# Performance work log

Hardware: AMD Instinct MI355X
Metric: run time of the kernel (lower is better)

The kernel has to match this reference:

```python
import jax, jax.numpy as jnp
import numpy as np

N_FREQ = 128
N_SPACE = 3
DIS_DIM = 2 * N_FREQ * N_SPACE  # 768


def sin_emb(x):
    # x: [E, 3] -> [E, 768]; frequencies = 2*pi*arange(n_freq) as in DiffCSP SinusoidsEmbedding
    freq = 2.0 * jnp.pi * jnp.arange(N_FREQ, dtype=x.dtype)
    e = (x[..., None] * freq).reshape(x.shape[0], N_SPACE * N_FREQ)
    return jnp.concatenate([jnp.sin(e), jnp.cos(e)], axis=-1)


def layer_norm(x, g, b, eps=1e-5):
    m = jnp.mean(x, axis=-1, keepdims=True)
    v = jnp.var(x, axis=-1, keepdims=True)
    return (x - m) * jax.lax.rsqrt(v + eps) * g + b


def setup_inputs() -> dict:
    key = jax.random.key(0)
    ks = jax.random.split(key, 16)
    N, E, B, H = 10000, 200000, 50, 512
    E_IN = 2 * H + DIS_DIM + 6  # 1798
    s = 0.02
    return {
        "node_features": jax.random.normal(ks[0], (N, H), jnp.float32),
        "lattices": jax.random.normal(ks[1], (B, 6), jnp.float32),
        "edge_index": jax.random.randint(ks[2], (2, E), 0, N),
        "edge2graph": jax.random.randint(ks[3], (E,), 0, B),
        "frac_diff": jax.random.uniform(ks[4], (E, 3), jnp.float32),
        "num_atoms": jax.random.randint(ks[5], (B,), 1, 200),
        "ln_gamma": jnp.ones((H,), jnp.float32),
        "ln_beta": jnp.zeros((H,), jnp.float32),
        "W_e1": jax.random.normal(ks[6], (E_IN, H), jnp.float32) * s,
        "b_e1": jnp.zeros((H,), jnp.float32),
        "W_e2": jax.random.normal(ks[7], (H, H), jnp.float32) * s,
        "b_e2": jnp.zeros((H,), jnp.float32),
        "W_n1": jax.random.normal(ks[8], (2 * H, H), jnp.float32) * s,
        "b_n1": jnp.zeros((H,), jnp.float32),
        "W_n2": jax.random.normal(ks[9], (H, H), jnp.float32) * s,
        "b_n2": jnp.zeros((H,), jnp.float32),
    }


def reference(node_features, lattices, edge_index, edge2graph, frac_diff, num_atoms,
              ln_gamma, ln_beta, W_e1, b_e1, W_e2, b_e2, W_n1, b_n1, W_n2, b_n2):
    N = node_features.shape[0]
    # pre-LN (ln=True): residual uses raw input
    h = layer_norm(node_features, ln_gamma, ln_beta)
    # edge model: gather + concat + 2-layer MLP with SiLU
    hi = h[edge_index[0]]
    hj = h[edge_index[1]]
    fd = sin_emb(frac_diff)
    lat_e = lattices.reshape(lattices.shape[0], -1)[edge2graph]
    e_in = jnp.concatenate([hi, hj, lat_e, fd], axis=1)  # [E, 1798]
    e = jax.nn.silu(e_in @ W_e1 + b_e1)
    e = jax.nn.silu(e @ W_e2 + b_e2)
    # node model: scatter-mean over edge source + 2-layer MLP
    agg = jax.ops.segment_sum(e, edge_index[0], num_segments=N)
    cnt = jax.ops.segment_sum(jnp.ones((e.shape[0],), e.dtype), edge_index[0], num_segments=N)
    agg = agg / jnp.maximum(cnt, 1.0)[:, None]
    n_in = jnp.concatenate([h, agg], axis=1)  # [N, 1024]
    o = jax.nn.silu(n_in @ W_n1 + b_n1)
    o = jax.nn.silu(o @ W_n2 + b_n2)
    return node_features + o
```

## Files before the change

### kernel.cpp

```cpp
#include <hip/hip_runtime.h>
#include <hip/hip_bf16.h>


#include <type_traits>

typedef __attribute__((ext_vector_type(8))) short bfrag;
typedef __attribute__((ext_vector_type(4))) float ffrag;

#define DEVI __device__ __forceinline__

constexpr int N_NODES = 10000;
constexpr int N_EDGES = 200000;
constexpr int HD      = 512;
constexpr int NT      = HD / 16;
constexpr int SLABW   = 520;
constexpr int KSTR    = NT * 64 * 8;

DEVI float silu_f(float v) {
    return v * __builtin_amdgcn_rcpf(1.0f + __expf(-v));
}

DEVI ushort f2bf(float f) {
    unsigned u = __float_as_uint(f);
    unsigned r = (u + 0x7fffu + ((u >> 16) & 1u)) >> 16;
    return (ushort)r;
}
DEVI float bf2f(ushort v) { return __uint_as_float((unsigned)v << 16); }

DEVI int cperm(int col) {
    return (col & ~63) | ((col & 15) << 2) | ((col >> 4) & 3);
}

__global__ void wswz_kernel(const float* __restrict__ W, ushort* __restrict__ dst,
                            int Kp, int mode) {
    int fid = blockIdx.x * blockDim.x + threadIdx.x;
    int total = (Kp / 32) * NT * 64;
    if (fid >= total) return;
    int l  = fid & 63;
    int nn = (fid >> 6) & 31;
    int kk = fid >> 11;
    int col = nn * 16 + (l & 15);
    int kb  = kk * 32 + (l >> 4) * 8;
    union { ushort u16[8]; uint4 u4; } v;
    for (int j = 0; j < 8; ++j) {
        int krow = kb + j;
        int src;
        if (mode == 3) {
            int d = krow >> 8, rm = krow & 255, k = rm >> 1;
            src = ((rm & 1) ? 1414 : 1030) + d * 128 + k;
        } else if (mode == 1) {
            src = (krow & ~63) | ((krow & 3) << 4) | ((krow >> 2) & 15);
        } else {
            src = krow;
        }
        v.u16[j] = f2bf(W[(size_t)src * HD + col]);
    }
    *(uint4*)(dst + (size_t)fid * 8) = v.u4;
}

__global__ void ln_kernel(const float* __restrict__ x, const float* __restrict__ g,
                          const float* __restrict__ b, ushort* __restrict__ h) {
    __shared__ float wred[8];
    __shared__ float mb[2];
    int row = blockIdx.x;
    int t = threadIdx.x;
    const float* xr = x + (size_t)row * HD;
    float2 xv = *(const float2*)(xr + 2 * t);
    float s = xv.x + xv.y, qq = xv.x * xv.x + xv.y * xv.y;
    for (int o = 32; o; o >>= 1) { s += __shfl_down(s, o); qq += __shfl_down(qq, o); }
    int w = t >> 6, l = t & 63;
    if (l == 0) { wred[w] = s; wred[w + 4] = qq; }
    __syncthreads();
    if (t == 0) {
        float S = wred[0] + wred[1] + wred[2] + wred[3];
        float Q = wred[4] + wred[5] + wred[6] + wred[7];
        float m = S * (1.0f / HD);
        float v = Q * (1.0f / HD) - m * m;
        mb[0] = m; mb[1] = rsqrtf(v + 1e-5f);
    }
    __syncthreads();
    float m = mb[0], rs = mb[1];
    float2 gv = *(const float2*)(g + 2 * t);
    float2 bv = *(const float2*)(b + 2 * t);
    __hip_bfloat162 o2 = __float22bfloat162_rn(
        float2{(xv.x - m) * rs * gv.x + bv.x, (xv.y - m) * rs * gv.y + bv.y});
    *(__hip_bfloat162*)(h + (size_t)row * HD + 2 * t) = o2;
}

__global__ void latb_kernel(const float* __restrict__ latt, const float* __restrict__ W_e1,
                            const float* __restrict__ b1, float* __restrict__ LATBp) {
    int g = blockIdx.x;
    int t = threadIdx.x;
    float a = b1[t];
    for (int c = 0; c < 6; ++c)
        a += latt[g * 6 + c] * W_e1[(size_t)(1024 + c) * HD + t];
    LATBp[(size_t)g * HD + cperm(t)] = a;
}

__global__ void zero_kernel(int* __restrict__ c32, float4* __restrict__ agg4) {
    int i = blockIdx.x * 256 + threadIdx.x;
    if (i < N_NODES) c32[i] = 0;
    agg4[i] = float4{0.f, 0.f, 0.f, 0.f};
}

__global__ void hist_kernel(const int* __restrict__ eidx, int* __restrict__ cnt32) {
    int e = blockIdx.x * 256 + threadIdx.x;
    if (e < N_EDGES) atomicAdd(&cnt32[eidx[e]], 1);
}

__global__ void scan_kernel(const int* __restrict__ cnt32, int* __restrict__ row_ptr,
                            int* __restrict__ cursor) {
    __shared__ int buf[1024];
    int t = threadIdx.x;
    int base = t * 10;
    int loc[10]; int s = 0;
    for (int i = 0; i < 10; ++i) {
        int idx = base + i;
        int v = (idx < N_NODES) ? cnt32[idx] : 0;
        loc[i] = s; s += v;
    }
    buf[t] = s; __syncthreads();
    for (int off = 1; off < 1024; off <<= 1) {
        int v = 0; if (t >= off) v = buf[t - off];
        __syncthreads();
        buf[t] += v; __syncthreads();
    }
    int excl = buf[t] - s;
    for (int i = 0; i < 10; ++i) {
        int idx = base + i;
        if (idx < N_NODES) { int p = excl + loc[i]; row_ptr[idx] = p; cursor[idx] = p; }
    }
    if (t == 0) row_ptr[N_NODES] = N_EDGES;
}

__global__ void csr_fill(const int* __restrict__ eidx, int* __restrict__ cursor,
                         int* __restrict__ ebuf) {
    int e = blockIdx.x * 256 + threadIdx.x;
    if (e >= N_EDGES) return;
    int pos = atomicAdd(&cursor[eidx[e]], 1);
    ebuf[pos] = e;
}

__global__ void aggdiv_kernel(const float* __restrict__ agg, const int* __restrict__ rp,
                              ushort* __restrict__ aggb) {
    int i = blockIdx.x * 256 + threadIdx.x;
    int row = i >> 8;
    int deg = rp[row + 1] - rp[row];
    float rc = __builtin_amdgcn_rcpf((float)max(deg, 1));
    float2 v = *(const float2*)(agg + (size_t)i * 2);
    *(__hip_bfloat162*)(aggb + (size_t)i * 2) =
        __float22bfloat162_rn(float2{v.x * rc, v.y * rc});
}

__global__ void sentinel_kernel(float* o, int n) {
    int i = blockIdx.x * 256 + threadIdx.x;
    if (i < n) o[i] = 123456789.0f;
}

template <int KTN, int MT>
DEVI void kloop_rot(ffrag (&acc)[MT][4], const ushort* sl, const ushort* bp0,
                    int ml, int q) {
    bfrag b_[4];
    const ushort* bp = bp0;
    #pragma unroll
    for (int n = 0; n < 4; ++n) b_[n] = *(const bfrag*)(bp + n * 512);
    #pragma unroll
    for (int p = 0; p < KTN; ++p) {
        bfrag a_[MT];
        #pragma unroll
        for (int m = 0; m < MT; ++m)
            a_[m] = *(const bfrag*)&sl[(16 * m + ml) * SLABW + p * 32 + q * 8];
        const ushort* bpn = bp + KSTR;
        #pragma unroll
        for (int n = 0; n < 4; ++n) {
            #pragma unroll
            for (int m = 0; m < MT; ++m)
                acc[m][n] = __builtin_amdgcn_mfma_f32_16x16x32_bf16(a_[m], b_[n], acc[m][n], 0, 0, 0);
            if (p + 1 < KTN) b_[n] = *(const bfrag*)(bpn + n * 512);
        }
        bp = bpn;
    }
}

__global__ __launch_bounds__(512, 4) void hab_gemm(
    const ushort* __restrict__ h, const ushort* __restrict__ w1a_s,
    const ushort* __restrict__ w1b_s, ushort* __restrict__ HAp,
    ushort* __restrict__ HBp) {

    __shared__ __align__(16) ushort slab[32 * SLABW];
    const int t = threadIdx.x;
    const int w = t >> 6;
    const int l = t & 63;
    const int q = l >> 4;
    const int ml = l & 15;
    const int rowbase = blockIdx.x * 32;
    const ushort* Bswz = blockIdx.y ? w1b_s : w1a_s;
    ushort* out = blockIdx.y ? HBp : HAp;

    for (int j = 0; j < 4; ++j) {
        int rr = w * 4 + j;
        int row = rowbase + rr;
        if (row >= N_NODES) row = N_NODES - 1;
        *(uint4*)&slab[rr * SLABW + l * 8] =
            *(const uint4*)(h + (size_t)row * HD + l * 8);
    }
    __syncthreads();

    ffrag acc[2][4];
    for (int m = 0; m < 2; ++m)
        for (int n = 0; n < 4; ++n)
            acc[m][n] = (ffrag){0.f, 0.f, 0.f, 0.f};

    kloop_rot<16, 2>(acc, slab, Bswz + ((size_t)(w << 2) * 64 + l) * 8, ml, q);

    for (int m = 0; m < 2; ++m)
        for (int rr = 0; rr < 4; ++rr) {
            int grow = rowbase + 16 * m + 4 * q + rr;
            if (grow < N_NODES) {
                union { __hip_bfloat162 h2[2]; ushort4 u4; } pk;
                pk.h2[0] = __float22bfloat162_rn(float2{acc[m][0][rr], acc[m][1][rr]});
                pk.h2[1] = __float22bfloat162_rn(float2{acc[m][2][rr], acc[m][3][rr]});
                *(ushort4*)(out + (size_t)grow * HD + w * 64 + ml * 4) = pk.u4;
            }
        }
}

__global__ __launch_bounds__(512, 4) void edge_mlp(
    const ushort* __restrict__ HAp,   const ushort* __restrict__ HBp,
    const float* __restrict__ LATBp,  const ushort* __restrict__ w1c,
    const ushort* __restrict__ w2s,   const float* __restrict__ b2,
    float* __restrict__ agg,
    const int* __restrict__ edge_index, const int* __restrict__ e2g,
    const float* __restrict__ frac_diff, const int* __restrict__ ebuf) {

    __shared__ __align__(16) ushort slab[64 * SLABW];
    __shared__ int   ssrc[64];
    __shared__ int   sdst[64];
    __shared__ int   sgrp[64];
    __shared__ float sfd[64 * 3];

    const int t = threadIdx.x;
    const int w = t >> 6;
    const int l = t & 63;
    const int q = l >> 4;
    const int ml = l & 15;
    const int rowbase = blockIdx.x * 64;

    if (t < 64) {
        int eid = ebuf[rowbase + t];
        ssrc[t] = edge_index[eid];
        sdst[t] = edge_index[N_EDGES + eid];
        sgrp[t] = e2g[eid];
        for (int c = 0; c < 3; ++c) sfd[t * 3 + c] = frac_diff[(size_t)eid * 3 + c];
    }
    __syncthreads();

    ffrag acc[4][4];
    {
        const int cb = w * 64 + ml * 4;
        for (int m = 0; m < 4; ++m)
            for (int rr = 0; rr < 4; ++rr) {
                int rowl = 16 * m + 4 * q + rr;
                ushort4 a4 = *(const ushort4*)(HAp + (size_t)ssrc[rowl] * HD + cb);
                ushort4 h4 = *(const ushort4*)(HBp + (size_t)sdst[rowl] * HD + cb);
                float4  l4 = *(const float4*)(LATBp + (size_t)sgrp[rowl] * HD + cb);
                acc[m][0][rr] = bf2f(a4.x) + bf2f(h4.x) + l4.x;
                acc[m][1][rr] = bf2f(a4.y) + bf2f(h4.y) + l4.y;
                acc[m][2][rr] = bf2f(a4.z) + bf2f(h4.z) + l4.z;
                acc[m][3][rr] = bf2f(a4.w) + bf2f(h4.w) + l4.w;
            }
    }

    const int r  = t >> 3;
    const int c0 = (t & 7) * 4;
    float fd3[3] = { sfd[r * 3 + 0], sfd[r * 3 + 1], sfd[r * 3 + 2] };

    auto stage = [&](int phase) {
        float s = 0.f, c = 0.f, sx = 0.f, cx = 0.f, s16 = 0.f, c16 = 0.f;
        int dcur = -1;
        #pragma unroll
        for (int i = 0; i < 12; ++i) {
            int cc = c0 + 32 * i;
            int cp = phase * 384 + cc;
            int d = cp >> 8;
            if (d != dcur) {
                dcur = d;
                float x = fd3[d];
                float rx = __builtin_amdgcn_fractf(x);
                sx  = __builtin_amdgcn_sinf(rx);
                cx  = __builtin_amdgcn_cosf(rx);
                float r16 = __builtin_amdgcn_fractf(16.0f * x);
                s16 = __builtin_amdgcn_sinf(r16);
                c16 = __builtin_amdgcn_cosf(r16);
                int k0 = (cp & 255) >> 1;
                float r0 = __builtin_amdgcn_fractf((float)k0 * x);
                s = __builtin_amdgcn_sinf(r0);
                c = __builtin_amdgcn_cosf(r0);
            } else {
                float ns = s * c16 + c * s16;
                float nc = c * c16 - s * s16;
                s = ns; c = nc;
            }
            float s1 = s * cx + c * sx;
            float c1 = c * cx - s * sx;
            union { __hip_bfloat162 h2[2]; ushort4 u4; } pk;
            pk.h2[0] = __float22bfloat162_rn(float2{s, c});
            pk.h2[1] = __float22bfloat162_rn(float2{s1, c1});
            *(ushort4*)&slab[r * SLABW + cc] = pk.u4;
        }
    };

    const ushort* bpw1 = w1c + ((size_t)(w << 2) * 64 + l) * 8;
    const ushort* bpw2 = w2s + ((size_t)(w << 2) * 64 + l) * 8;

    stage(0);
    __syncthreads();
    kloop_rot<12, 4>(acc, slab, bpw1, ml, q);
    __syncthreads();
    stage(1);
    __syncthreads();
    kloop_rot<12, 4>(acc, slab, bpw1 + (size_t)12 * KSTR, ml, q);
    __syncthreads();

    for (int m = 0; m < 4; ++m)
        for (int rr = 0; rr < 4; ++rr) {
            int rowl = 16 * m + 4 * q + rr;
            union { __hip_bfloat162 h2[2]; ushort4 u4; } pk;
            pk.h2[0] = __float22bfloat162_rn(
                float2{silu_f(acc[m][0][rr]), silu_f(acc[m][1][rr])});
            pk.h2[1] = __float22bfloat162_rn(
                float2{silu_f(acc[m][2][rr]), silu_f(acc[m][3][rr])});
            *(ushort4*)&slab[rowl * SLABW + w * 64 + ml * 4] = pk.u4;
        }
    for (int m = 0; m < 4; ++m)
        for (int n = 0; n < 4; ++n)
            acc[m][n] = (ffrag){0.f, 0.f, 0.f, 0.f};
    __syncthreads();

    kloop_rot<16, 4>(acc, slab, bpw2, ml, q);

    float* fs = (float*)slab;
    for (int hh = 0; hh < 2; ++hh) {
        __syncthreads();
        if ((w >> 2) == hh) {
            for (int n = 0; n < 4; ++n) {
                int cg = w * 64 + n * 16 + ml;
                int lc = cg - hh * 256;
                float bv = b2[cg];
                for (int m = 0; m < 4; ++m)
                    for (int rr = 0; rr < 4; ++rr) {
                        int rowl = 16 * m + 4 * q + rr;
                        fs[rowl * 256 + lc] = silu_f(acc[m][n][rr] + bv);
                    }
            }
        }
        __syncthreads();
        if (t < 256) {
            int col = hh * 256 + t;
            int cur = ssrc[0];
            float run = 0.f;
            for (int rr2 = 0; rr2 < 64; ++rr2) {
                int nd = ssrc[rr2];
                if (nd != cur) {
                    unsafeAtomicAdd(&agg[(size_t)cur * HD + col], run);
                    run = 0.f; cur = nd;
                }
                run += fs[rr2 * 256 + t];
            }
            unsafeAtomicAdd(&agg[(size_t)cur * HD + col], run);
        }
    }
}

__global__ __launch_bounds__(512, 4) void node_mlp(
    const ushort* __restrict__ h,     const ushort* __restrict__ aggb,
    const ushort* __restrict__ wn1s,  const ushort* __restrict__ wn2s,
    const float* __restrict__ b1,     const float* __restrict__ b2,
    const float* __restrict__ nf,     float* __restrict__ out) {

    __shared__ __align__(16) ushort slab[32 * SLABW];

    const int t = threadIdx.x;
    const int w = t >> 6;
    const int l = t & 63;
    const int q = l >> 4;
    const int ml = l & 15;
    const int rowbase = blockIdx.x * 32;

    ffrag acc[2][4];
    for (int m = 0; m < 2; ++m)
        for (int n = 0; n < 4; ++n)
            acc[m][n] = (ffrag){0.f, 0.f, 0.f, 0.f};

    auto load_rows = [&](const ushort* base) {
        for (int j = 0; j < 4; ++j) {
            int rr = w * 4 + j;
            int row = rowbase + rr;
            if (row >= N_NODES) row = N_NODES - 1;
            *(uint4*)&slab[rr * SLABW + l * 8] =
                *(const uint4*)(base + (size_t)row * HD + l * 8);
        }
    };
    const ushort* bp1 = wn1s + ((size_t)(w << 2) * 64 + l) * 8;
    const ushort* bp2 = wn2s + ((size_t)(w << 2) * 64 + l) * 8;

    load_rows(h);                        __syncthreads();
    kloop_rot<16, 2>(acc, slab, bp1, ml, q);
    __syncthreads();
    load_rows(aggb);                     __syncthreads();
    kloop_rot<16, 2>(acc, slab, bp1 + (size_t)16 * KSTR, ml, q);
    __syncthreads();

    {
        float bv[4];
        for (int n = 0; n < 4; ++n) bv[n] = b1[w * 64 + n * 16 + ml];
        for (int m = 0; m < 2; ++m)
            for (int rr = 0; rr < 4; ++rr) {
                int rowl = 16 * m + 4 * q + rr;
                union { __hip_bfloat162 h2[2]; ushort4 u4; } pk;
                pk.h2[0] = __float22bfloat162_rn(
                    float2{silu_f(acc[m][0][rr] + bv[0]), silu_f(acc[m][1][rr] + bv[1])});
                pk.h2[1] = __float22bfloat162_rn(
                    float2{silu_f(acc[m][2][rr] + bv[2]), silu_f(acc[m][3][rr] + bv[3])});
                *(ushort4*)&slab[rowl * SLABW + w * 64 + ml * 4] = pk.u4;
            }
    }
    for (int m = 0; m < 2; ++m)
        for (int n = 0; n < 4; ++n)
            acc[m][n] = (ffrag){0.f, 0.f, 0.f, 0.f};
    __syncthreads();

    kloop_rot<16, 2>(acc, slab, bp2, ml, q);

    for (int n = 0; n < 4; ++n) {
        int cg = w * 64 + n * 16 + ml;
        float bv = b2[cg];
        for (int m = 0; m < 2; ++m)
            for (int rr = 0; rr < 4; ++rr) {
                int rowl = 16 * m + 4 * q + rr;
                int row = rowbase + rowl;
                if (row < N_NODES) {
                    float v = silu_f(acc[m][n][rr] + bv);
                    out[(size_t)row * HD + cg] = nf[(size_t)row * HD + cg] + v;
                }
            }
    }
}

extern "C" void kernel_launch(void* const* d_in, const int* in_sizes, int n_in,
                              void* d_out, int out_size, void* d_ws, size_t ws_size,
                              hipStream_t stream) {
    const float* nf      = (const float*)d_in[0];
    const float* latt    = (const float*)d_in[1];
    const int*   eidx    = (const int*)d_in[2];
    const int*   e2g     = (const int*)d_in[3];
    const float* fd      = (const float*)d_in[4];
    const float* ln_g    = (const float*)d_in[6];
    const float* ln_b    = (const float*)d_in[7];
    const float* W_e1    = (const float*)d_in[8];
    const float* b_e1    = (const float*)d_in[9];
    const float* W_e2    = (const float*)d_in[10];
    const float* b_e2    = (const float*)d_in[11];
    const float* W_n1    = (const float*)d_in[12];
    const float* b_n1    = (const float*)d_in[13];
    const float* W_n2    = (const float*)d_in[14];
    const float* b_n2    = (const float*)d_in[15];
    float* out = (float*)d_out;

    auto al = [](size_t x) { return (x + 511) & ~(size_t)511; };
    size_t off_h    = 0;                         size_t sz_h    = (size_t)N_NODES * HD * 2;
    size_t off_w1a  = al(off_h + sz_h);          size_t sz_w1a  = (size_t)HD * HD * 2;
    size_t off_w1b  = al(off_w1a + sz_w1a);      size_t sz_w1b  = (size_t)HD * HD * 2;
    size_t off_w1c  = al(off_w1b + sz_w1b);      size_t sz_w1c  = (size_t)768 * HD * 2;
    size_t off_w2   = al(off_w1c + sz_w1c);      size_t sz_w2   = (size_t)HD * HD * 2;
    size_t off_wn1  = al(off_w2 + sz_w2);        size_t sz_wn1  = (size_t)2 * HD * HD * 2;
    size_t off_wn2  = al(off_wn1 + sz_wn1);      size_t sz_wn2  = (size_t)HD * HD * 2;
    size_t off_ha   = al(off_wn2 + sz_wn2);      size_t sz_ha   = (size_t)N_NODES * HD * 2;
    size_t off_hb   = al(off_ha + sz_ha);        size_t sz_hb   = (size_t)N_NODES * HD * 2;
    size_t off_lb   = al(off_hb + sz_hb);        size_t sz_lb   = (size_t)50 * HD * 4;
    size_t off_agb  = al(off_lb + sz_lb);        size_t sz_agb  = (size_t)N_NODES * HD * 2;
    size_t off_c32  = al(off_agb + sz_agb);      size_t sz_c32  = (size_t)N_NODES * 4;
    size_t off_cur  = al(off_c32 + sz_c32);      size_t sz_cur  = (size_t)N_NODES * 4;
    size_t off_rp   = al(off_cur + sz_cur);      size_t sz_rp   = (size_t)(N_NODES + 1) * 4;
    size_t off_ebuf = al(off_rp + sz_rp);        size_t sz_ebuf = (size_t)N_EDGES * 4;
    size_t off_agg  = al(off_ebuf + sz_ebuf);    size_t sz_agg  = (size_t)N_NODES * HD * 4;
    size_t need     = off_agg + sz_agg;

    if (ws_size < need) {
        sentinel_kernel<<<(out_size + 255) / 256, 256, 0, stream>>>(out, out_size);
        return;
    }

    char* ws = (char*)d_ws;
    ushort* h     = (ushort*)(ws + off_h);
    ushort* w1a_s = (ushort*)(ws + off_w1a);
    ushort* w1b_s = (ushort*)(ws + off_w1b);
    ushort* w1c_s = (ushort*)(ws + off_w1c);
    ushort* w2s   = (ushort*)(ws + off_w2);
    ushort* wn1s  = (ushort*)(ws + off_wn1);
    ushort* wn2s  = (ushort*)(ws + off_wn2);
    ushort* HAp   = (ushort*)(ws + off_ha);
    ushort* HBp   = (ushort*)(ws + off_hb);
    float*  LATBp = (float*)(ws + off_lb);
    ushort* aggb  = (ushort*)(ws + off_agb);
    int*    c32   = (int*)(ws + off_c32);
    int*    cur   = (int*)(ws + off_cur);
    int*    rp    = (int*)(ws + off_rp);
    int*    ebuf  = (int*)(ws + off_ebuf);
    float*  agg   = (float*)(ws + off_agg);

    zero_kernel<<<(N_NODES * HD / 4) / 256, 256, 0, stream>>>(c32, (float4*)agg);
    wswz_kernel<<<(HD / 32) * NT * 64 / 256, 256, 0, stream>>>(W_e1, w1a_s, HD, 0);
    wswz_kernel<<<(HD / 32) * NT * 64 / 256, 256, 0, stream>>>(W_e1 + (size_t)HD * HD, w1b_s, HD, 0);
    wswz_kernel<<<(768 / 32) * NT * 64 / 256, 256, 0, stream>>>(W_e1, w1c_s, 768, 3);
    wswz_kernel<<<(HD / 32) * NT * 64 / 256, 256, 0, stream>>>(W_e2, w2s, HD, 1);
    wswz_kernel<<<(2 * HD / 32) * NT * 64 / 256, 256, 0, stream>>>(W_n1, wn1s, 2 * HD, 0);
    wswz_kernel<<<(HD / 32) * NT * 64 / 256, 256, 0, stream>>>(W_n2, wn2s, HD, 1);
    latb_kernel<<<50, 512, 0, stream>>>(latt, W_e1, b_e1, LATBp);

    hist_kernel<<<(N_EDGES + 255) / 256, 256, 0, stream>>>(eidx, c32);
    scan_kernel<<<1, 1024, 0, stream>>>(c32, rp, cur);
    csr_fill<<<(N_EDGES + 255) / 256, 256, 0, stream>>>(eidx, cur, ebuf);

    ln_kernel<<<N_NODES, 256, 0, stream>>>(nf, ln_g, ln_b, h);
    hab_gemm<<<dim3(313, 2), 512, 0, stream>>>(h, w1a_s, w1b_s, HAp, HBp);

    edge_mlp<<<N_EDGES / 64, 512, 0, stream>>>(
        HAp, HBp, LATBp, w1c_s, w2s, b_e2, agg, eidx, e2g, fd, ebuf);

    aggdiv_kernel<<<(N_NODES * HD / 2) / 256, 256, 0, stream>>>(agg, rp, aggb);

    int nblocks = (N_NODES + 31) / 32;
    node_mlp<<<nblocks, 512, 0, stream>>>(h, aggb, wn1s, wn2s, b_n1, b_n2, nf, out);
}
```

Measured before the change: 561.5 us.

## Vectorize edge epilogue stores with permuted columns and split segment reduction over all threads

In the edge MLP epilogue, each lane now writes four adjacent columns as one float4 into a padded shared staging buffer. This makes the aggregated edge features land in a permuted column order. The node MLP weight swizzle gets a new mode that permutes the agg half of W_n1 rows to match, so results stay correct. The segmented scatter-sum now uses all 512 threads, each covering half of the 64 rows, instead of 256 threads covering all 64, and bias loads are hoisted out of the loop. The intent is fewer shared-memory store instructions and bank conflicts and more parallel reduction. The cost is possibly extra global atomics where a node's run of edges crosses the row split.

```diff
diff --git a/kernel.cpp b/kernel.cpp
--- a/kernel.cpp
+++ b/kernel.cpp
@@ -14,6 +14,7 @@
 constexpr int HD      = 512;
 constexpr int NT      = HD / 16;
 constexpr int SLABW   = 520;
+constexpr int FSW     = 260;
 constexpr int KSTR    = NT * 64 * 8;
 
 DEVI float silu_f(float v) {
@@ -50,6 +51,9 @@
             src = ((rm & 1) ? 1414 : 1030) + d * 128 + k;
         } else if (mode == 1) {
             src = (krow & ~63) | ((krow & 3) << 4) | ((krow >> 2) & 15);
+        } else if (mode == 2) {
+            src = (krow < 512) ? krow
+                : ((krow & ~63) | ((krow & 3) << 4) | ((krow >> 2) & 15));
         } else {
             src = krow;
         }
@@ -340,34 +344,40 @@
     kloop_rot<16, 4>(acc, slab, bpw2, ml, q);
 
     float* fs = (float*)slab;
+    float bv0 = b2[w * 64 + 0 * 16 + ml];
+    float bv1 = b2[w * 64 + 1 * 16 + ml];
+    float bv2 = b2[w * 64 + 2 * 16 + ml];
+    float bv3 = b2[w * 64 + 3 * 16 + ml];
     for (int hh = 0; hh < 2; ++hh) {
         __syncthreads();
         if ((w >> 2) == hh) {
-            for (int n = 0; n < 4; ++n) {
-                int cg = w * 64 + n * 16 + ml;
-                int lc = cg - hh * 256;
-                float bv = b2[cg];
-                for (int m = 0; m < 4; ++m)
-                    for (int rr = 0; rr < 4; ++rr) {
-                        int rowl = 16 * m + 4 * q + rr;
-                        fs[rowl * 256 + lc] = silu_f(acc[m][n][rr] + bv);
-                    }
-            }
+            int lcb = w * 64 + ml * 4 - hh * 256;
+            for (int m = 0; m < 4; ++m)
+                for (int rr = 0; rr < 4; ++rr) {
+                    int rowl = 16 * m + 4 * q + rr;
+                    float4 v = float4{silu_f(acc[m][0][rr] + bv0),
+                                      silu_f(acc[m][1][rr] + bv1),
+                                      silu_f(acc[m][2][rr] + bv2),
+                                      silu_f(acc[m][3][rr] + bv3)};
+                    *(float4*)&fs[rowl * FSW + lcb] = v;
+                }
         }
         __syncthreads();
-        if (t < 256) {
-            int col = hh * 256 + t;
-            int cur = ssrc[0];
+        {
+            int col = t & 255;
+            int r0 = (t >> 8) * 32;
+            int cur = ssrc[r0];
             float run = 0.f;
-            for (int rr2 = 0; rr2 < 64; ++rr2) {
+            for (int j = 0; j < 32; ++j) {
+                int rr2 = r0 + j;
                 int nd = ssrc[rr2];
                 if (nd != cur) {
-                    unsafeAtomicAdd(&agg[(size_t)cur * HD + col], run);
+                    unsafeAtomicAdd(&agg[(size_t)cur * HD + hh * 256 + col], run);
                     run = 0.f; cur = nd;
                 }
-                run += fs[rr2 * 256 + t];
+                run += fs[rr2 * FSW + col];
             }
-            unsafeAtomicAdd(&agg[(size_t)cur * HD + col], run);
+            unsafeAtomicAdd(&agg[(size_t)cur * HD + hh * 256 + col], run);
         }
     }
 }
@@ -514,7 +524,7 @@
     wswz_kernel<<<(HD / 32) * NT * 64 / 256, 256, 0, stream>>>(W_e1 + (size_t)HD * HD, w1b_s, HD, 0);
     wswz_kernel<<<(768 / 32) * NT * 64 / 256, 256, 0, stream>>>(W_e1, w1c_s, 768, 3);
     wswz_kernel<<<(HD / 32) * NT * 64 / 256, 256, 0, stream>>>(W_e2, w2s, HD, 1);
-    wswz_kernel<<<(2 * HD / 32) * NT * 64 / 256, 256, 0, stream>>>(W_n1, wn1s, 2 * HD, 0);
+    wswz_kernel<<<(2 * HD / 32) * NT * 64 / 256, 256, 0, stream>>>(W_n1, wn1s, 2 * HD, 2);
     wswz_kernel<<<(HD / 32) * NT * 64 / 256, 256, 0, stream>>>(W_n2, wn2s, HD, 1);
     latb_kernel<<<50, 512, 0, stream>>>(latt, W_e1, b_e1, LATBp);
 
```

New measurement: 538.0 us. 1.04x faster.
